# Performance work log

Hardware: AMD Instinct MI355X
Metric: run time of the kernel (lower is better)

## Reference

```python
import jax, jax.numpy as jnp
import numpy as np

BN_EPS = 1e-5


def _l2norm(v, eps=1e-12):
    return v / (jnp.linalg.norm(v) + eps)


def _sn_weight(W, u):
    # torch spectral_norm, n_power_iterations=1; u, v detached, grad flows via W
    v = _l2norm(W.T @ u)
    u_new = _l2norm(W @ v)
    u_new = jax.lax.stop_gradient(u_new)
    v = jax.lax.stop_gradient(v)
    sigma = u_new @ (W @ v)
    return W / sigma


def setup_inputs() -> dict:
    key = jax.random.key(0)
    ks = jax.random.split(key, 8)
    N, E, nfeat, nhid = 65536, 1048576, 64, 128
    x = jax.random.normal(ks[0], (N, nfeat), dtype=jnp.float32)
    edge_index = jax.random.randint(ks[1], (2, E), 0, N, dtype=jnp.int64)
    s1 = 1.0 / np.sqrt(nfeat)
    s2 = 1.0 / np.sqrt(nhid)
    W1 = jax.random.uniform(ks[2], (nhid, nfeat), jnp.float32, -s1, s1)
    b1 = jax.random.uniform(ks[3], (nhid,), jnp.float32, -s1, s1)
    u1 = jax.random.normal(ks[4], (nhid,), dtype=jnp.float32)
    gamma = jnp.ones((nhid,), jnp.float32)
    beta = jnp.zeros((nhid,), jnp.float32)
    W2 = jax.random.uniform(ks[5], (nhid, nhid), jnp.float32, -s2, s2)
    b2 = jax.random.uniform(ks[6], (nhid,), jnp.float32, -s2, s2)
    u2 = jax.random.normal(ks[7], (nhid,), dtype=jnp.float32)
    return {"x": x, "edge_index": edge_index, "W1": W1, "b1": b1, "u1": u1,
            "gamma": gamma, "beta": beta, "W2": W2, "b2": b2, "u2": u2}


def reference(x, edge_index, W1, b1, u1, gamma, beta, W2, b2, u2):
    N = x.shape[0]
    src, dst = edge_index[0], edge_index[1]
    # GIN neighbor sum aggregation: agg[i] = sum_{(j->i)} x[j]
    agg = jax.ops.segment_sum(x[src], dst, num_segments=N)
    h = x + agg  # (1 + eps) * x + agg, eps = 0
    # MLP: SN-Linear -> ReLU -> BatchNorm1d (training stats) -> SN-Linear
    h = h @ _sn_weight(W1, u1).T + b1
    h = jax.nn.relu(h)
    mean = jnp.mean(h, axis=0)
    var = jnp.var(h, axis=0)  # biased, as torch BN uses for normalization
    h = (h - mean) * jax.lax.rsqrt(var + BN_EPS) * gamma + beta
    out = h @ _sn_weight(W2, u2).T + b2
    return out
```

## Files before the change

kernel.cpp:

```cpp
#include <hip/hip_runtime.h>


#define BN_EPS 1e-5f
#define NB   512
#define CAP  2816

typedef float f4 __attribute__((ext_vector_type(4)));
typedef short bf8 __attribute__((ext_vector_type(8)));

__device__ inline short f2bf(float f) {
    unsigned u = __float_as_uint(f);
    u = u + 0x7fffu + ((u >> 16) & 1u);
    return (short)(u >> 16);
}
__device__ inline float bf2f(unsigned short u) {
    return __uint_as_float((unsigned)u << 16);
}
__device__ inline unsigned pk2(float a, float b) {
    return (unsigned)(unsigned short)f2bf(a) |
           ((unsigned)(unsigned short)f2bf(b) << 16);
}

__global__ __launch_bounds__(256) void kprep(const float* __restrict__ x,
                                             unsigned* __restrict__ xbf2,
                                             const float* __restrict__ W1,
                                             short* __restrict__ w1bf,
                                             int* __restrict__ zbase) {
    int bid = blockIdx.x;
    int t = threadIdx.x;
    if (bid < 2048) {
        int i = bid * 256 + t;
        const float4* xp = (const float4*)x;
        float4 a = xp[2 * i], b = xp[2 * i + 1];
        uint4 o = {pk2(a.x, a.y), pk2(a.z, a.w), pk2(b.x, b.y), pk2(b.z, b.w)};
        ((uint4*)xbf2)[i] = o;
    } else if (bid < 2052) {
        int base = (bid - 2048) * 2048 + t * 8;
        float4 a = *(const float4*)(W1 + base);
        float4 b = *(const float4*)(W1 + base + 4);
        uint4 o = {pk2(a.x, a.y), pk2(a.z, a.w), pk2(b.x, b.y), pk2(b.z, b.w)};
        *(uint4*)(w1bf + base) = o;
    } else {
        zbase[t] = 0; zbase[256 + t] = 0; zbase[512 + t] = 0;
    }
}

__global__ __launch_bounds__(512) void kbin(const int* __restrict__ ei, int E,
                                            int* __restrict__ gcount,
                                            unsigned* __restrict__ pairs,
                                            const float* __restrict__ W1,
                                            const float* __restrict__ u1,
                                            const float* __restrict__ W2,
                                            const float* __restrict__ u2,
                                            float* __restrict__ sinv) {
    __shared__ int hist[512];
    __shared__ int sbase[512];
    __shared__ int cur[512];
    __shared__ int gofs[512];
    __shared__ unsigned stage[4096];
    int t = threadIdx.x;

    if (blockIdx.x < 256) {
        hist[t] = 0;
        __syncthreads();

        const uint4* s4 = (const uint4*)ei + blockIdx.x * 1024;
        const uint4* d4 = (const uint4*)(ei + E) + blockIdx.x * 1024;
        unsigned pk[8];
#pragma unroll
        for (int i = 0; i < 2; i++) {
            int idx = i * 512 + t;
            uint4 sv = s4[idx];
            uint4 dv = d4[idx];
            pk[i * 4 + 0] = ((dv.x >> 7) << 23) | (sv.x << 7) | (dv.x & 127u);
            pk[i * 4 + 1] = ((dv.y >> 7) << 23) | (sv.y << 7) | (dv.y & 127u);
            pk[i * 4 + 2] = ((dv.z >> 7) << 23) | (sv.z << 7) | (dv.z & 127u);
            pk[i * 4 + 3] = ((dv.w >> 7) << 23) | (sv.w << 7) | (dv.w & 127u);
            atomicAdd(&hist[dv.x >> 7], 1);
            atomicAdd(&hist[dv.y >> 7], 1);
            atomicAdd(&hist[dv.z >> 7], 1);
            atomicAdd(&hist[dv.w >> 7], 1);
        }
        __syncthreads();

        int cntb = hist[t];
        for (int o = 1; o < 512; o <<= 1) {
            int v = (t >= o) ? hist[t - o] : 0;
            __syncthreads();
            hist[t] += v;
            __syncthreads();
        }
        int excl = hist[t] - cntb;
        sbase[t] = excl;
        cur[t] = excl;
        __syncthreads();

#pragma unroll
        for (int i = 0; i < 8; i++) {
            int p = atomicAdd(&cur[pk[i] >> 23], 1);
            stage[p] = pk[i];
        }
        __syncthreads();

        gofs[t] = atomicAdd(&gcount[t], cntb);
        __syncthreads();

#pragma unroll
        for (int i = 0; i < 8; i++) {
            int p = i * 512 + t;
            unsigned v = stage[p];
            int b = (int)(v >> 23);
            int li = p - sbase[b];
            pairs[(size_t)b * CAP + gofs[b] + li] = v & 0x7FFFFFu;
        }
    } else {
        float* red = (float*)stage;
        float* v   = (float*)hist;
        float* sq  = (float*)sbase;

        {
            int j = t & 63, q = t >> 6;
            float s = 0.f;
            for (int i = q * 16; i < q * 16 + 16; i++) s += W1[i * 64 + j] * u1[i];
            red[t] = s;
        }
        __syncthreads();
        if (t < 64) {
            float vj = 0.f;
#pragma unroll
            for (int g = 0; g < 8; g++) vj += red[g * 64 + t];
            v[t] = vj; sq[t] = vj * vj;
        }
        __syncthreads();
        for (int s2 = 32; s2 > 0; s2 >>= 1) {
            if (t < s2) sq[t] += sq[t + s2];
            __syncthreads();
        }
        if (t < 64) v[t] = v[t] / (sqrtf(sq[0]) + 1e-12f);
        __syncthreads();
        {
            int r = t >> 2, h = t & 3;
            const float4* wr = (const float4*)(W1 + r * 64 + h * 16);
            const float4* vv = (const float4*)v + h * 4;
            float s = 0.f;
#pragma unroll
            for (int k = 0; k < 4; k++) {
                float4 a = wr[k]; float4 b = vv[k];
                s += a.x * b.x + a.y * b.y + a.z * b.z + a.w * b.w;
            }
            red[t] = s;
        }
        __syncthreads();
        if (t < 128) {
            float tr = (red[4 * t] + red[4 * t + 1]) + (red[4 * t + 2] + red[4 * t + 3]);
            sq[t] = tr * tr;
        }
        __syncthreads();
        for (int s2 = 64; s2 > 0; s2 >>= 1) {
            if (t < s2) sq[t] += sq[t + s2];
            __syncthreads();
        }
        if (t == 0) { float nt2 = sq[0]; sinv[0] = (sqrtf(nt2) + 1e-12f) / nt2; }
        __syncthreads();

        {
            int j = t & 127, q = t >> 7;
            float s = 0.f;
            for (int i = q * 32; i < q * 32 + 32; i++) s += W2[i * 128 + j] * u2[i];
            red[t] = s;
        }
        __syncthreads();
        if (t < 128) {
            float vj = (red[t] + red[128 + t]) + (red[256 + t] + red[384 + t]);
            v[t] = vj; sq[t] = vj * vj;
        }
        __syncthreads();
        for (int s2 = 64; s2 > 0; s2 >>= 1) {
            if (t < s2) sq[t] += sq[t + s2];
            __syncthreads();
        }
        if (t < 128) v[t] = v[t] / (sqrtf(sq[0]) + 1e-12f);
        __syncthreads();
        {
            int r = t >> 2, h = t & 3;
            const float4* wr = (const float4*)(W2 + r * 128 + h * 32);
            const float4* vv = (const float4*)v + h * 8;
            float s = 0.f;
#pragma unroll
            for (int k = 0; k < 8; k++) {
                float4 a = wr[k]; float4 b = vv[k];
                s += a.x * b.x + a.y * b.y + a.z * b.z + a.w * b.w;
            }
            red[t] = s;
        }
        __syncthreads();
        if (t < 128) {
            float tr = (red[4 * t] + red[4 * t + 1]) + (red[4 * t + 2] + red[4 * t + 3]);
            sq[t] = tr * tr;
        }
        __syncthreads();
        for (int s2 = 64; s2 > 0; s2 >>= 1) {
            if (t < s2) sq[t] += sq[t + s2];
            __syncthreads();
        }
        if (t == 0) { float nt2 = sq[0]; sinv[1] = (sqrtf(nt2) + 1e-12f) / nt2; }
    }
}

__global__ __launch_bounds__(512) void kaggs(const unsigned* __restrict__ pairs,
                                             const int* __restrict__ gcount,
                                             const unsigned* __restrict__ xbf2,
                                             unsigned* __restrict__ hbf2) {
    __shared__ unsigned ep[CAP];
    __shared__ unsigned short sorted[CAP];
    __shared__ int hist[128];
    __shared__ int offs[128];
    __shared__ int cur[128];
    int t = threadIdx.x;
    int b = blockIdx.x;
    int cnt = gcount[b];

    {
        const uint4* gp4 = (const uint4*)(pairs + (size_t)b * CAP);
        int cnt4 = (cnt + 3) >> 2;
        for (int j = t; j < cnt4; j += 512) ((uint4*)ep)[j] = gp4[j];
    }
    if (t < 128) hist[t] = 0;
    __syncthreads();
    for (int j = t; j < cnt; j += 512) atomicAdd(&hist[ep[j] & 127u], 1);
    __syncthreads();
    int cntb = (t < 128) ? hist[t] : 0;
    for (int o = 1; o < 128; o <<= 1) {
        int v = (t < 128 && t >= o) ? hist[t - o] : 0;
        __syncthreads();
        if (t < 128) hist[t] += v;
        __syncthreads();
    }
    if (t < 128) { offs[t] = hist[t] - cntb; cur[t] = hist[t] - cntb; }
    __syncthreads();
    for (int j = t; j < cnt; j += 512) {
        unsigned v = ep[j];
        int p = atomicAdd(&cur[v & 127u], 1);
        sorted[p] = (unsigned short)(v >> 7);
    }
    __syncthreads();

    int w = t >> 6;
    int lane = t & 63;
    int h = lane >> 5;
    int l = lane & 31;

#pragma unroll
    for (int ni = 0; ni < 16; ni++) {
        int n = w * 16 + ni;
        int g = b * 128 + n;
        int beg = offs[n], end = hist[n];
        float a0 = 0.f, a1 = 0.f, b0 = 0.f, b1 = 0.f;
        float c0 = 0.f, c1 = 0.f, d0 = 0.f, d1 = 0.f;
        int j = beg + h;
        for (; j + 6 < end; j += 8) {
            int s0 = sorted[j];
            int s1 = sorted[j + 2];
            int s2 = sorted[j + 4];
            int s3 = sorted[j + 6];
            unsigned v0 = xbf2[(size_t)s0 * 32 + l];
            unsigned v1 = xbf2[(size_t)s1 * 32 + l];
            unsigned v2 = xbf2[(size_t)s2 * 32 + l];
            unsigned v3 = xbf2[(size_t)s3 * 32 + l];
            a0 += bf2f((unsigned short)v0); a1 += bf2f((unsigned short)(v0 >> 16));
            b0 += bf2f((unsigned short)v1); b1 += bf2f((unsigned short)(v1 >> 16));
            c0 += bf2f((unsigned short)v2); c1 += bf2f((unsigned short)(v2 >> 16));
            d0 += bf2f((unsigned short)v3); d1 += bf2f((unsigned short)(v3 >> 16));
        }
        for (; j < end; j += 2) {
            unsigned v = xbf2[(size_t)sorted[j] * 32 + l];
            a0 += bf2f((unsigned short)v); a1 += bf2f((unsigned short)(v >> 16));
        }
        a0 = (a0 + b0) + (c0 + d0);
        a1 = (a1 + b1) + (c1 + d1);
        a0 += __shfl_xor(a0, 32);
        a1 += __shfl_xor(a1, 32);
        unsigned xs = xbf2[(size_t)g * 32 + l];
        a0 += bf2f((unsigned short)xs);
        a1 += bf2f((unsigned short)(xs >> 16));
        if (h == 0) hbf2[(size_t)g * 32 + l] = pk2(a0, a1);
    }
}

__global__ __launch_bounds__(256) void k3_gemm1(const short* __restrict__ hbf,
                                                const short* __restrict__ w1bf,
                                                const float* __restrict__ b1,
                                                const float* __restrict__ sinv,
                                                short* __restrict__ h1bf,
                                                float* __restrict__ bnacc) {
    __shared__ short u[16384];
    __shared__ float red1[512], red2[512];
    int t = threadIdx.x;
    int n0 = blockIdx.x * 128;

    const bf8* hsrc = (const bf8*)(hbf + (size_t)n0 * 64);
    const bf8* wsrc = (const bf8*)w1bf;
#pragma unroll
    for (int i = 0; i < 4; i++) {
        int idx = i * 256 + t;
        int row = idx >> 3, c = idx & 7;
        int cs = c ^ (row & 7);
        *(bf8*)&u[row * 64 + cs * 8] = hsrc[idx];
    }
#pragma unroll
    for (int i = 0; i < 4; i++) {
        int idx = i * 256 + t;
        int row = idx >> 3, c = idx & 7;
        int cs = c ^ (row & 7);
        *(bf8*)&u[8192 + row * 64 + cs * 8] = wsrc[idx];
    }
    __syncthreads();

    int w = t >> 6;
    int l15 = t & 15, quad = (t & 63) >> 4;

    f4 acc[2][8];
#pragma unroll
    for (int mt = 0; mt < 2; mt++)
#pragma unroll
        for (int nt = 0; nt < 8; nt++) acc[mt][nt] = (f4){0.f, 0.f, 0.f, 0.f};

#pragma unroll
    for (int ks = 0; ks < 2; ks++) {
        bf8 a[2], b[8];
#pragma unroll
        for (int mt = 0; mt < 2; mt++) {
            int node = w * 32 + mt * 16 + l15;
            int cs = (ks * 4 + quad) ^ (node & 7);
            a[mt] = *(const bf8*)&u[node * 64 + cs * 8];
        }
#pragma unroll
        for (int nt = 0; nt < 8; nt++) {
            int o = nt * 16 + l15;
            int cs = (ks * 4 + quad) ^ (o & 7);
            b[nt] = *(const bf8*)&u[8192 + o * 64 + cs * 8];
        }
#pragma unroll
        for (int mt = 0; mt < 2; mt++)
#pragma unroll
            for (int nt = 0; nt < 8; nt++)
                acc[mt][nt] = __builtin_amdgcn_mfma_f32_16x16x32_bf16(
                    a[mt], b[nt], acc[mt][nt], 0, 0, 0);
    }

    float s1 = sinv[0];
    float b1v[8];
#pragma unroll
    for (int nt = 0; nt < 8; nt++) b1v[nt] = b1[nt * 16 + l15];

#pragma unroll
    for (int nt = 0; nt < 8; nt++) {
        float s = 0.f, q = 0.f;
#pragma unroll
        for (int mt = 0; mt < 2; mt++)
#pragma unroll
            for (int r = 0; r < 4; r++) {
                float v = fmaxf(fmaf(acc[mt][nt][r], s1, b1v[nt]), 0.f);
                acc[mt][nt][r] = v;
                s += v; q += v * v;
            }
        s += __shfl_xor(s, 16); s += __shfl_xor(s, 32);
        q += __shfl_xor(q, 16); q += __shfl_xor(q, 32);
        if (quad == 0) {
            red1[w * 128 + nt * 16 + l15] = s;
            red2[w * 128 + nt * 16 + l15] = q;
        }
    }
    __syncthreads();

#pragma unroll
    for (int mt = 0; mt < 2; mt++)
#pragma unroll
        for (int nt = 0; nt < 8; nt++) {
            int col = nt * 16 + l15;
#pragma unroll
            for (int r = 0; r < 4; r++) {
                int node = w * 32 + mt * 16 + quad * 4 + r;
                int cs = (col >> 3) ^ (node & 15);
                u[node * 128 + cs * 8 + (col & 7)] = f2bf(acc[mt][nt][r]);
            }
        }
    __syncthreads();

    short* dst = h1bf + (size_t)n0 * 128;
#pragma unroll
    for (int i = 0; i < 8; i++) {
        int idx = i * 256 + t;
        int row = idx >> 4, c = idx & 15;
        int cs = c ^ (row & 15);
        *(bf8*)&dst[idx * 8] = *(const bf8*)&u[row * 128 + cs * 8];
    }
    if (t < 128) {
        float s = red1[t] + red1[128 + t] + red1[256 + t] + red1[384 + t];
        float q = red2[t] + red2[128 + t] + red2[256 + t] + red2[384 + t];
        atomicAdd(&bnacc[t], s);
        atomicAdd(&bnacc[128 + t], q);
    }
}

__global__ __launch_bounds__(128) void k4_fold(const float* __restrict__ bnacc,
                                               int N,
                                               const float* __restrict__ gamma,
                                               const float* __restrict__ beta,
                                               const float* __restrict__ W2,
                                               const float* __restrict__ b2,
                                               const float* __restrict__ sinv,
                                               short* __restrict__ W2fbf,
                                               float* __restrict__ b2f) {
    __shared__ float a_s[128], c_s[128];
    int t = threadIdx.x;
    {
        float mean = bnacc[t] / (float)N;
        float var = bnacc[t + 128] / (float)N - mean * mean;
        float rstd = rsqrtf(var + BN_EPS);
        float a = rstd * gamma[t];
        a_s[t] = a;
        c_s[t] = beta[t] - mean * a;
    }
    __syncthreads();
    float s2 = sinv[1];
    float accb = 0.f;
    for (int j = 0; j < 128; j++) {
        float w = W2[t * 128 + j] * s2;
        W2fbf[t * 128 + j] = f2bf(w * a_s[j]);
        accb += w * c_s[j];
    }
    b2f[t] = b2[t] + accb;
}

__global__ __launch_bounds__(256) void k5_gemm2(const short* __restrict__ h1bf,
                                                const short* __restrict__ w2fbf,
                                                const float* __restrict__ b2f,
                                                float* __restrict__ out) {
    __shared__ short s5[32768];
    int t = threadIdx.x;
    int n0 = blockIdx.x * 128;

    const bf8* hsrc = (const bf8*)(h1bf + (size_t)n0 * 128);
    const bf8* wsrc = (const bf8*)w2fbf;
#pragma unroll
    for (int i = 0; i < 8; i++) {
        int idx = i * 256 + t;
        int row = idx >> 4, c = idx & 15;
        int cs = c ^ (row & 15);
        *(bf8*)&s5[row * 128 + cs * 8] = hsrc[idx];
    }
#pragma unroll
    for (int i = 0; i < 8; i++) {
        int idx = i * 256 + t;
        int row = idx >> 4, c = idx & 15;
        int cs = c ^ (row & 15);
        *(bf8*)&s5[16384 + row * 128 + cs * 8] = wsrc[idx];
    }
    __syncthreads();

    int w = t >> 6;
    int l15 = t & 15, quad = (t & 63) >> 4;

    f4 acc[2][8];
#pragma unroll
    for (int mt = 0; mt < 2; mt++)
#pragma unroll
        for (int nt = 0; nt < 8; nt++) acc[mt][nt] = (f4){0.f, 0.f, 0.f, 0.f};

#pragma unroll
    for (int ks = 0; ks < 4; ks++) {
        bf8 a[2], b[8];
#pragma unroll
        for (int mt = 0; mt < 2; mt++) {
            int node = w * 32 + mt * 16 + l15;
            int cs = (ks * 4 + quad) ^ (node & 15);
            a[mt] = *(const bf8*)&s5[node * 128 + cs * 8];
        }
#pragma unroll
        for (int nt = 0; nt < 8; nt++) {
            int o = nt * 16 + l15;
            int cs = (ks * 4 + quad) ^ (o & 15);
            b[nt] = *(const bf8*)&s5[16384 + o * 128 + cs * 8];
        }
#pragma unroll
        for (int mt = 0; mt < 2; mt++)
#pragma unroll
            for (int nt = 0; nt < 8; nt++)
                acc[mt][nt] = __builtin_amdgcn_mfma_f32_16x16x32_bf16(
                    a[mt], b[nt], acc[mt][nt], 0, 0, 0);
    }

    float b2v[8];
#pragma unroll
    for (int nt = 0; nt < 8; nt++) b2v[nt] = b2f[nt * 16 + l15];

#pragma unroll
    for (int mt = 0; mt < 2; mt++)
#pragma unroll
        for (int nt = 0; nt < 8; nt++)
#pragma unroll
            for (int r = 0; r < 4; r++) {
                int node = n0 + w * 32 + mt * 16 + quad * 4 + r;
                out[(size_t)node * 128 + nt * 16 + l15] = acc[mt][nt][r] + b2v[nt];
            }
}

extern "C" void kernel_launch(void* const* d_in, const int* in_sizes, int n_in,
                              void* d_out, int out_size, void* d_ws, size_t ws_size,
                              hipStream_t stream) {
    const float* x     = (const float*)d_in[0];
    const int*   ei    = (const int*)d_in[1];
    const float* W1    = (const float*)d_in[2];
    const float* b1    = (const float*)d_in[3];
    const float* u1    = (const float*)d_in[4];
    const float* gamma = (const float*)d_in[5];
    const float* beta  = (const float*)d_in[6];
    const float* W2    = (const float*)d_in[7];
    const float* b2    = (const float*)d_in[8];
    const float* u2    = (const float*)d_in[9];
    float* out = (float*)d_out;

    int N = in_sizes[0] / 64;
    int E = in_sizes[1] / 2;
    int nblk = N / 128;

    char* ws = (char*)d_ws;
    size_t off = 0;
    short* hbf     = (short*)(ws + off); off += (size_t)N * 64 * 2;
    char*  region2 = ws + off;           off += (size_t)N * 128 * 2;
    unsigned* pairs = (unsigned*)region2;
    unsigned short* xbf = (unsigned short*)(region2 + (size_t)NB * CAP * 4);
    short*    h1bf  = (short*)region2;
    int*   gcount  = (int*)(ws + off);   off += 512 * 4;
    float* bnacc   = (float*)(ws + off); off += 256 * 4;
    float* sinv    = (float*)(ws + off); off += 16 * 4;
    float* b2f     = (float*)(ws + off); off += 128 * 4;
    short* w1bf    = (short*)(ws + off); off += 128 * 64 * 2;
    short* w2fbf   = (short*)(ws + off); off += 128 * 128 * 2;

    kprep<<<2053, 256, 0, stream>>>(x, (unsigned*)xbf, W1, w1bf, gcount);
    kbin<<<257, 512, 0, stream>>>(ei, E, gcount, pairs, W1, u1, W2, u2, sinv);
    kaggs<<<NB, 512, 0, stream>>>(pairs, gcount, (const unsigned*)xbf,
                                  (unsigned*)hbf);
    k3_gemm1<<<nblk, 256, 0, stream>>>(hbf, w1bf, b1, sinv, h1bf, bnacc);
    k4_fold<<<1, 128, 0, stream>>>(bnacc, N, gamma, beta, W2, b2, sinv, w2fbf, b2f);
    k5_gemm2<<<nblk, 256, 0, stream>>>(h1bf, w2fbf, b2f, out);
}
```

Before: 179.8 us.

## Fuse aggregation with GEMM1 and BN fold with GEMM2, cut launches

Collapses six launches into a memset plus three kernels. The bf16 conversion of x and W1 moves into the binning kernel. Neighbor aggregation now feeds GEMM1 directly through shared memory, so the intermediate h buffer never goes to global memory. The BN/weight fold is recomputed per block inside GEMM2, and the bf16 h1 tile is staged in the output buffer's own block region. This removes launch overhead and one global round trip, at the cost of redundant W2 folding in every block and higher LDS/register use in the fused aggregation kernel.

Result: faster. 164.0 us (-8.8%).

```diff
diff --git a/kernel.cpp b/kernel.cpp
--- a/kernel.cpp
+++ b/kernel.cpp
@@ -21,51 +21,31 @@
            ((unsigned)(unsigned short)f2bf(b) << 16);
 }
 
-__global__ __launch_bounds__(256) void kprep(const float* __restrict__ x,
-                                             unsigned* __restrict__ xbf2,
-                                             const float* __restrict__ W1,
-                                             short* __restrict__ w1bf,
-                                             int* __restrict__ zbase) {
-    int bid = blockIdx.x;
-    int t = threadIdx.x;
-    if (bid < 2048) {
-        int i = bid * 256 + t;
-        const float4* xp = (const float4*)x;
-        float4 a = xp[2 * i], b = xp[2 * i + 1];
-        uint4 o = {pk2(a.x, a.y), pk2(a.z, a.w), pk2(b.x, b.y), pk2(b.z, b.w)};
-        ((uint4*)xbf2)[i] = o;
-    } else if (bid < 2052) {
-        int base = (bid - 2048) * 2048 + t * 8;
-        float4 a = *(const float4*)(W1 + base);
-        float4 b = *(const float4*)(W1 + base + 4);
-        uint4 o = {pk2(a.x, a.y), pk2(a.z, a.w), pk2(b.x, b.y), pk2(b.z, b.w)};
-        *(uint4*)(w1bf + base) = o;
-    } else {
-        zbase[t] = 0; zbase[256 + t] = 0; zbase[512 + t] = 0;
-    }
-}
-
-__global__ __launch_bounds__(512) void kbin(const int* __restrict__ ei, int E,
-                                            int* __restrict__ gcount,
-                                            unsigned* __restrict__ pairs,
-                                            const float* __restrict__ W1,
-                                            const float* __restrict__ u1,
-                                            const float* __restrict__ W2,
-                                            const float* __restrict__ u2,
-                                            float* __restrict__ sinv) {
+__global__ __launch_bounds__(512) void k1_bin(const int* __restrict__ ei, int E,
+                                              int* __restrict__ gcount,
+                                              unsigned* __restrict__ pairs,
+                                              const float* __restrict__ x,
+                                              unsigned* __restrict__ xbf2,
+                                              const float* __restrict__ W1,
+                                              short* __restrict__ w1bf,
+                                              const float* __restrict__ u1,
+                                              const float* __restrict__ W2,
+                                              const float* __restrict__ u2,
+                                              float* __restrict__ sinv) {
     __shared__ int hist[512];
     __shared__ int sbase[512];
     __shared__ int cur[512];
     __shared__ int gofs[512];
     __shared__ unsigned stage[4096];
     int t = threadIdx.x;
-
-    if (blockIdx.x < 256) {
+    int bid = blockIdx.x;
+
+    if (bid < 256) {
         hist[t] = 0;
         __syncthreads();
 
-        const uint4* s4 = (const uint4*)ei + blockIdx.x * 1024;
-        const uint4* d4 = (const uint4*)(ei + E) + blockIdx.x * 1024;
+        const uint4* s4 = (const uint4*)ei + bid * 1024;
+        const uint4* d4 = (const uint4*)(ei + E) + bid * 1024;
         unsigned pk[8];
 #pragma unroll
         for (int i = 0; i < 2; i++) {
@@ -113,7 +93,25 @@
             int li = p - sbase[b];
             pairs[(size_t)b * CAP + gofs[b] + li] = v & 0x7FFFFFu;
         }
+    } else if (bid < 512) {
+        int cb = bid - 256;
+        const float4* xp = (const float4*)x;
+#pragma unroll
+        for (int k = 0; k < 4; k++) {
+            int i = cb * 2048 + k * 512 + t;
+            float4 a = xp[2 * i], b = xp[2 * i + 1];
+            uint4 o = {pk2(a.x, a.y), pk2(a.z, a.w), pk2(b.x, b.y), pk2(b.z, b.w)};
+            ((uint4*)xbf2)[i] = o;
+        }
     } else {
+#pragma unroll
+        for (int k = 0; k < 2; k++) {
+            int idx = k * 512 + t;
+            const float4* wp = (const float4*)W1;
+            float4 a = wp[2 * idx], b = wp[2 * idx + 1];
+            uint4 o = {pk2(a.x, a.y), pk2(a.z, a.w), pk2(b.x, b.y), pk2(b.z, b.w)};
+            ((uint4*)w1bf)[idx] = o;
+        }
         float* red = (float*)stage;
         float* v   = (float*)hist;
         float* sq  = (float*)sbase;
@@ -207,19 +205,26 @@
     }
 }
 
-__global__ __launch_bounds__(512) void kaggs(const unsigned* __restrict__ pairs,
-                                             const int* __restrict__ gcount,
-                                             const unsigned* __restrict__ xbf2,
-                                             unsigned* __restrict__ hbf2) {
-    __shared__ unsigned ep[CAP];
+__global__ __launch_bounds__(512) void k2_agg_gemm1(
+        const unsigned* __restrict__ pairs,
+        const int* __restrict__ gcount,
+        const unsigned* __restrict__ xbf2,
+        const short* __restrict__ w1bf,
+        const float* __restrict__ b1,
+        const float* __restrict__ sinv,
+        char* __restrict__ outbase,
+        float* __restrict__ bnacc) {
+    __shared__ short u[16384];
     __shared__ unsigned short sorted[CAP];
     __shared__ int hist[128];
     __shared__ int offs[128];
     __shared__ int cur[128];
+    __shared__ float red1[1024], red2[1024];
     int t = threadIdx.x;
     int b = blockIdx.x;
     int cnt = gcount[b];
 
+    unsigned* ep = (unsigned*)u;
     {
         const uint4* gp4 = (const uint4*)(pairs + (size_t)b * CAP);
         int cnt4 = (cnt + 3) >> 2;
@@ -249,13 +254,14 @@
     int lane = t & 63;
     int h = lane >> 5;
     int l = lane & 31;
+    float hr0[16], hr1[16];
 
 #pragma unroll
     for (int ni = 0; ni < 16; ni++) {
         int n = w * 16 + ni;
         int g = b * 128 + n;
         int beg = offs[n], end = hist[n];
-        float a0 = 0.f, a1 = 0.f, b0 = 0.f, b1 = 0.f;
+        float a0 = 0.f, a1 = 0.f, b0 = 0.f, b1r = 0.f;
         float c0 = 0.f, c1 = 0.f, d0 = 0.f, d1 = 0.f;
         int j = beg + h;
         for (; j + 6 < end; j += 8) {
@@ -268,7 +274,7 @@
             unsigned v2 = xbf2[(size_t)s2 * 32 + l];
             unsigned v3 = xbf2[(size_t)s3 * 32 + l];
             a0 += bf2f((unsigned short)v0); a1 += bf2f((unsigned short)(v0 >> 16));
-            b0 += bf2f((unsigned short)v1); b1 += bf2f((unsigned short)(v1 >> 16));
+            b0 += bf2f((unsigned short)v1); b1r += bf2f((unsigned short)(v1 >> 16));
             c0 += bf2f((unsigned short)v2); c1 += bf2f((unsigned short)(v2 >> 16));
             d0 += bf2f((unsigned short)v3); d1 += bf2f((unsigned short)(v3 >> 16));
         }
@@ -277,93 +283,72 @@
             a0 += bf2f((unsigned short)v); a1 += bf2f((unsigned short)(v >> 16));
         }
         a0 = (a0 + b0) + (c0 + d0);
-        a1 = (a1 + b1) + (c1 + d1);
+        a1 = (a1 + b1r) + (c1 + d1);
         a0 += __shfl_xor(a0, 32);
         a1 += __shfl_xor(a1, 32);
         unsigned xs = xbf2[(size_t)g * 32 + l];
         a0 += bf2f((unsigned short)xs);
         a1 += bf2f((unsigned short)(xs >> 16));
-        if (h == 0) hbf2[(size_t)g * 32 + l] = pk2(a0, a1);
-    }
-}
-
-__global__ __launch_bounds__(256) void k3_gemm1(const short* __restrict__ hbf,
-                                                const short* __restrict__ w1bf,
-                                                const float* __restrict__ b1,
-                                                const float* __restrict__ sinv,
-                                                short* __restrict__ h1bf,
-                                                float* __restrict__ bnacc) {
-    __shared__ short u[16384];
-    __shared__ float red1[512], red2[512];
-    int t = threadIdx.x;
-    int n0 = blockIdx.x * 128;
-
-    const bf8* hsrc = (const bf8*)(hbf + (size_t)n0 * 64);
-    const bf8* wsrc = (const bf8*)w1bf;
-#pragma unroll
-    for (int i = 0; i < 4; i++) {
-        int idx = i * 256 + t;
-        int row = idx >> 3, c = idx & 7;
-        int cs = c ^ (row & 7);
-        *(bf8*)&u[row * 64 + cs * 8] = hsrc[idx];
-    }
-#pragma unroll
-    for (int i = 0; i < 4; i++) {
-        int idx = i * 256 + t;
-        int row = idx >> 3, c = idx & 7;
-        int cs = c ^ (row & 7);
-        *(bf8*)&u[8192 + row * 64 + cs * 8] = wsrc[idx];
-    }
-    __syncthreads();
-
-    int w = t >> 6;
-    int l15 = t & 15, quad = (t & 63) >> 4;
-
-    f4 acc[2][8];
-#pragma unroll
-    for (int mt = 0; mt < 2; mt++)
-#pragma unroll
-        for (int nt = 0; nt < 8; nt++) acc[mt][nt] = (f4){0.f, 0.f, 0.f, 0.f};
+        hr0[ni] = a0; hr1[ni] = a1;
+    }
+    __syncthreads();
+
+    if (h == 0) {
+#pragma unroll
+        for (int ni = 0; ni < 16; ni++) {
+            int n = w * 16 + ni;
+            int c = l >> 2;
+            int cs = c ^ (n & 7);
+            *(unsigned*)&u[n * 64 + cs * 8 + (l & 3) * 2] = pk2(hr0[ni], hr1[ni]);
+        }
+    }
+    {
+        const bf8* wsrc = (const bf8*)w1bf;
+#pragma unroll
+        for (int i = 0; i < 2; i++) {
+            int idx = i * 512 + t;
+            int row = idx >> 3, c = idx & 7;
+            int cs = c ^ (row & 7);
+            *(bf8*)&u[8192 + row * 64 + cs * 8] = wsrc[idx];
+        }
+    }
+    __syncthreads();
+
+    int l15 = lane & 15, quad = lane >> 4;
+    f4 acc[8];
+#pragma unroll
+    for (int nt = 0; nt < 8; nt++) acc[nt] = (f4){0.f, 0.f, 0.f, 0.f};
 
 #pragma unroll
     for (int ks = 0; ks < 2; ks++) {
-        bf8 a[2], b[8];
-#pragma unroll
-        for (int mt = 0; mt < 2; mt++) {
-            int node = w * 32 + mt * 16 + l15;
+        bf8 a, bfr[8];
+        {
+            int node = w * 16 + l15;
             int cs = (ks * 4 + quad) ^ (node & 7);
-            a[mt] = *(const bf8*)&u[node * 64 + cs * 8];
+            a = *(const bf8*)&u[node * 64 + cs * 8];
         }
 #pragma unroll
         for (int nt = 0; nt < 8; nt++) {
             int o = nt * 16 + l15;
             int cs = (ks * 4 + quad) ^ (o & 7);
-            b[nt] = *(const bf8*)&u[8192 + o * 64 + cs * 8];
-        }
-#pragma unroll
-        for (int mt = 0; mt < 2; mt++)
-#pragma unroll
-            for (int nt = 0; nt < 8; nt++)
-                acc[mt][nt] = __builtin_amdgcn_mfma_f32_16x16x32_bf16(
-                    a[mt], b[nt], acc[mt][nt], 0, 0, 0);
+            bfr[nt] = *(const bf8*)&u[8192 + o * 64 + cs * 8];
+        }
+#pragma unroll
+        for (int nt = 0; nt < 8; nt++)
+            acc[nt] = __builtin_amdgcn_mfma_f32_16x16x32_bf16(a, bfr[nt], acc[nt], 0, 0, 0);
     }
 
     float s1 = sinv[0];
-    float b1v[8];
-#pragma unroll
-    for (int nt = 0; nt < 8; nt++) b1v[nt] = b1[nt * 16 + l15];
-
 #pragma unroll
     for (int nt = 0; nt < 8; nt++) {
+        float bb = b1[nt * 16 + l15];
         float s = 0.f, q = 0.f;
 #pragma unroll
-        for (int mt = 0; mt < 2; mt++)
-#pragma unroll
-            for (int r = 0; r < 4; r++) {
-                float v = fmaxf(fmaf(acc[mt][nt][r], s1, b1v[nt]), 0.f);
-                acc[mt][nt][r] = v;
-                s += v; q += v * v;
-            }
+        for (int r = 0; r < 4; r++) {
+            float v = fmaxf(fmaf(acc[nt][r], s1, bb), 0.f);
+            acc[nt][r] = v;
+            s += v; q += v * v;
+        }
         s += __shfl_xor(s, 16); s += __shfl_xor(s, 32);
         q += __shfl_xor(q, 16); q += __shfl_xor(q, 32);
         if (quad == 0) {
@@ -374,93 +359,107 @@
     __syncthreads();
 
 #pragma unroll
-    for (int mt = 0; mt < 2; mt++)
-#pragma unroll
-        for (int nt = 0; nt < 8; nt++) {
-            int col = nt * 16 + l15;
-#pragma unroll
-            for (int r = 0; r < 4; r++) {
-                int node = w * 32 + mt * 16 + quad * 4 + r;
-                int cs = (col >> 3) ^ (node & 15);
-                u[node * 128 + cs * 8 + (col & 7)] = f2bf(acc[mt][nt][r]);
-            }
-        }
-    __syncthreads();
-
-    short* dst = h1bf + (size_t)n0 * 128;
-#pragma unroll
-    for (int i = 0; i < 8; i++) {
-        int idx = i * 256 + t;
+    for (int nt = 0; nt < 8; nt++) {
+        int col = nt * 16 + l15;
+#pragma unroll
+        for (int r = 0; r < 4; r++) {
+            int row = w * 16 + quad * 4 + r;
+            int cs = (col >> 3) ^ (row & 15);
+            u[row * 128 + cs * 8 + (col & 7)] = f2bf(acc[nt][r]);
+        }
+    }
+    __syncthreads();
+
+    bf8* dst = (bf8*)(outbase + (size_t)b * 65536);
+#pragma unroll
+    for (int i = 0; i < 4; i++) {
+        int idx = i * 512 + t;
         int row = idx >> 4, c = idx & 15;
         int cs = c ^ (row & 15);
-        *(bf8*)&dst[idx * 8] = *(const bf8*)&u[row * 128 + cs * 8];
+        dst[idx] = *(const bf8*)&u[row * 128 + cs * 8];
     }
     if (t < 128) {
-        float s = red1[t] + red1[128 + t] + red1[256 + t] + red1[384 + t];
-        float q = red2[t] + red2[128 + t] + red2[256 + t] + red2[384 + t];
+        float s = 0.f, q = 0.f;
+#pragma unroll
+        for (int g = 0; g < 8; g++) { s += red1[g * 128 + t]; q += red2[g * 128 + t]; }
         atomicAdd(&bnacc[t], s);
         atomicAdd(&bnacc[128 + t], q);
     }
 }
 
-__global__ __launch_bounds__(128) void k4_fold(const float* __restrict__ bnacc,
-                                               int N,
-                                               const float* __restrict__ gamma,
-                                               const float* __restrict__ beta,
-                                               const float* __restrict__ W2,
-                                               const float* __restrict__ b2,
-                                               const float* __restrict__ sinv,
-                                               short* __restrict__ W2fbf,
-                                               float* __restrict__ b2f) {
-    __shared__ float a_s[128], c_s[128];
+__global__ __launch_bounds__(256) void k3_fold_gemm2(
+        const float* __restrict__ bnacc, int N,
+        const float* __restrict__ gamma,
+        const float* __restrict__ beta,
+        const float* __restrict__ W2,
+        const float* __restrict__ b2,
+        const float* __restrict__ sinv,
+        char* __restrict__ outbase) {
+    __shared__ short s5[32768];
+    float* fs = (float*)s5;
     int t = threadIdx.x;
-    {
+    int b = blockIdx.x;
+
+    if (t < 128) {
         float mean = bnacc[t] / (float)N;
         float var = bnacc[t + 128] / (float)N - mean * mean;
         float rstd = rsqrtf(var + BN_EPS);
         float a = rstd * gamma[t];
-        a_s[t] = a;
-        c_s[t] = beta[t] - mean * a;
-    }
-    __syncthreads();
+        fs[t] = a;
+        fs[128 + t] = beta[t] - mean * a;
+    }
+    __syncthreads();
+
     float s2 = sinv[1];
-    float accb = 0.f;
-    for (int j = 0; j < 128; j++) {
-        float w = W2[t * 128 + j] * s2;
-        W2fbf[t * 128 + j] = f2bf(w * a_s[j]);
-        accb += w * c_s[j];
-    }
-    b2f[t] = b2[t] + accb;
-}
-
-__global__ __launch_bounds__(256) void k5_gemm2(const short* __restrict__ h1bf,
-                                                const short* __restrict__ w2fbf,
-                                                const float* __restrict__ b2f,
-                                                float* __restrict__ out) {
-    __shared__ short s5[32768];
-    int t = threadIdx.x;
-    int n0 = blockIdx.x * 128;
-
-    const bf8* hsrc = (const bf8*)(h1bf + (size_t)n0 * 128);
-    const bf8* wsrc = (const bf8*)w2fbf;
-#pragma unroll
-    for (int i = 0; i < 8; i++) {
-        int idx = i * 256 + t;
-        int row = idx >> 4, c = idx & 15;
-        int cs = c ^ (row & 15);
-        *(bf8*)&s5[row * 128 + cs * 8] = hsrc[idx];
-    }
-#pragma unroll
-    for (int i = 0; i < 8; i++) {
-        int idx = i * 256 + t;
-        int row = idx >> 4, c = idx & 15;
-        int cs = c ^ (row & 15);
-        *(bf8*)&s5[16384 + row * 128 + cs * 8] = wsrc[idx];
+    {
+        int o = t >> 1;
+        int jbase = (t & 1) * 64;
+        const float4* wr = (const float4*)(W2 + o * 128 + jbase);
+#pragma unroll
+        for (int k = 0; k < 8; k++) {
+            int c = (jbase >> 3) + k;
+            float4 a = wr[2 * k], bb = wr[2 * k + 1];
+            int j0 = jbase + k * 8;
+            bf8 v;
+            v[0] = f2bf(a.x * s2 * fs[j0 + 0]);
+            v[1] = f2bf(a.y * s2 * fs[j0 + 1]);
+            v[2] = f2bf(a.z * s2 * fs[j0 + 2]);
+            v[3] = f2bf(a.w * s2 * fs[j0 + 3]);
+            v[4] = f2bf(bb.x * s2 * fs[j0 + 4]);
+            v[5] = f2bf(bb.y * s2 * fs[j0 + 5]);
+            v[6] = f2bf(bb.z * s2 * fs[j0 + 6]);
+            v[7] = f2bf(bb.w * s2 * fs[j0 + 7]);
+            int cs = c ^ (o & 15);
+            *(bf8*)&s5[16384 + o * 128 + cs * 8] = v;
+        }
+    }
+    if (t < 128) {
+        float accb = 0.f;
+        for (int j = 0; j < 128; j++)
+            accb += W2[t * 128 + j] * s2 * fs[128 + j];
+        fs[256 + t] = b2[t] + accb;
     }
     __syncthreads();
 
     int w = t >> 6;
-    int l15 = t & 15, quad = (t & 63) >> 4;
+    int lane = t & 63;
+    int l15 = lane & 15, quad = lane >> 4;
+    float b2v[8];
+#pragma unroll
+    for (int nt = 0; nt < 8; nt++) b2v[nt] = fs[256 + nt * 16 + l15];
+    __syncthreads();
+
+    {
+        const bf8* hsrc = (const bf8*)(outbase + (size_t)b * 65536);
+#pragma unroll
+        for (int i = 0; i < 8; i++) {
+            int idx = i * 256 + t;
+            int row = idx >> 4, c = idx & 15;
+            int cs = c ^ (row & 15);
+            *(bf8*)&s5[row * 128 + cs * 8] = hsrc[idx];
+        }
+    }
+    __syncthreads();
 
     f4 acc[2][8];
 #pragma unroll
@@ -470,7 +469,7 @@
 
 #pragma unroll
     for (int ks = 0; ks < 4; ks++) {
-        bf8 a[2], b[8];
+        bf8 a[2], bfr[8];
 #pragma unroll
         for (int mt = 0; mt < 2; mt++) {
             int node = w * 32 + mt * 16 + l15;
@@ -481,28 +480,25 @@
         for (int nt = 0; nt < 8; nt++) {
             int o = nt * 16 + l15;
             int cs = (ks * 4 + quad) ^ (o & 15);
-            b[nt] = *(const bf8*)&s5[16384 + o * 128 + cs * 8];
+            bfr[nt] = *(const bf8*)&s5[16384 + o * 128 + cs * 8];
         }
 #pragma unroll
         for (int mt = 0; mt < 2; mt++)
 #pragma unroll
             for (int nt = 0; nt < 8; nt++)
                 acc[mt][nt] = __builtin_amdgcn_mfma_f32_16x16x32_bf16(
-                    a[mt], b[nt], acc[mt][nt], 0, 0, 0);
-    }
-
-    float b2v[8];
-#pragma unroll
-    for (int nt = 0; nt < 8; nt++) b2v[nt] = b2f[nt * 16 + l15];
-
+                    a[mt], bfr[nt], acc[mt][nt], 0, 0, 0);
+    }
+
+    float* out = (float*)(outbase + (size_t)b * 65536);
 #pragma unroll
     for (int mt = 0; mt < 2; mt++)
 #pragma unroll
         for (int nt = 0; nt < 8; nt++)
 #pragma unroll
             for (int r = 0; r < 4; r++) {
-                int node = n0 + w * 32 + mt * 16 + quad * 4 + r;
-                out[(size_t)node * 128 + nt * 16 + l15] = acc[mt][nt][r] + b2v[nt];
+                int row = w * 32 + mt * 16 + quad * 4 + r;
+                out[(size_t)row * 128 + nt * 16 + l15] = acc[mt][nt][r] + b2v[nt];
             }
 }
 
@@ -519,31 +515,24 @@
     const float* W2    = (const float*)d_in[7];
     const float* b2    = (const float*)d_in[8];
     const float* u2    = (const float*)d_in[9];
-    float* out = (float*)d_out;
 
     int N = in_sizes[0] / 64;
     int E = in_sizes[1] / 2;
-    int nblk = N / 128;
 
     char* ws = (char*)d_ws;
     size_t off = 0;
-    short* hbf     = (short*)(ws + off); off += (size_t)N * 64 * 2;
-    char*  region2 = ws + off;           off += (size_t)N * 128 * 2;
-    unsigned* pairs = (unsigned*)region2;
-    unsigned short* xbf = (unsigned short*)(region2 + (size_t)NB * CAP * 4);
-    short*    h1bf  = (short*)region2;
+    unsigned* pairs = (unsigned*)(ws + off); off += (size_t)NB * CAP * 4;
+    unsigned short* xbf = (unsigned short*)(ws + off); off += (size_t)N * 64 * 2;
     int*   gcount  = (int*)(ws + off);   off += 512 * 4;
     float* bnacc   = (float*)(ws + off); off += 256 * 4;
     float* sinv    = (float*)(ws + off); off += 16 * 4;
-    float* b2f     = (float*)(ws + off); off += 128 * 4;
     short* w1bf    = (short*)(ws + off); off += 128 * 64 * 2;
-    short* w2fbf   = (short*)(ws + off); off += 128 * 128 * 2;
-
-    kprep<<<2053, 256, 0, stream>>>(x, (unsigned*)xbf, W1, w1bf, gcount);
-    kbin<<<257, 512, 0, stream>>>(ei, E, gcount, pairs, W1, u1, W2, u2, sinv);
-    kaggs<<<NB, 512, 0, stream>>>(pairs, gcount, (const unsigned*)xbf,
-                                  (unsigned*)hbf);
-    k3_gemm1<<<nblk, 256, 0, stream>>>(hbf, w1bf, b1, sinv, h1bf, bnacc);
-    k4_fold<<<1, 128, 0, stream>>>(bnacc, N, gamma, beta, W2, b2, sinv, w2fbf, b2f);
-    k5_gemm2<<<nblk, 256, 0, stream>>>(h1bf, w2fbf, b2f, out);
-}
+
+    hipMemsetAsync(gcount, 0, 512 * 4 + 256 * 4, stream);
+    k1_bin<<<513, 512, 0, stream>>>(ei, E, gcount, pairs, x, (unsigned*)xbf,
+                                    W1, w1bf, u1, W2, u2, sinv);
+    k2_agg_gemm1<<<NB, 512, 0, stream>>>(pairs, gcount, (const unsigned*)xbf,
+                                         w1bf, b1, sinv, (char*)d_out, bnacc);
+    k3_fold_gemm2<<<NB, 256, 0, stream>>>(bnacc, N, gamma, beta, W2, b2, sinv,
+                                          (char*)d_out);
+}
```
